# Kernel optimization log

Hardware: AMD Instinct MI355X
Metric: run time of the kernel (lower is better)

Reference implementation:

```python
import jax, jax.numpy as jnp
import numpy as np

B, C, H, W = 8, 64, 256, 256
EPS = 1e-5


def setup_inputs() -> dict:
    key = jax.random.key(0)
    ks = jax.random.split(key, 8)
    s = 1.0 / np.sqrt(C)
    return {
        "x": jax.random.normal(ks[0], (B, C, H, W), dtype=jnp.float32),
        "Wq": jax.random.uniform(ks[1], (C, C), jnp.float32, -s, s),
        "bq": jnp.zeros((C,), jnp.float32),
        "Wk": jax.random.uniform(ks[2], (C, C), jnp.float32, -s, s),
        "bk": jnp.zeros((C,), jnp.float32),
        "Wv": jax.random.uniform(ks[3], (C, C), jnp.float32, -s, s),
        "bv": jnp.zeros((C,), jnp.float32),
        "gamma": jnp.ones((C,), jnp.float32),
        "beta": jnp.zeros((C,), jnp.float32),
        "running_mean": jnp.zeros((C,), jnp.float32),
        "running_var": jnp.ones((C,), jnp.float32),
        "alpha": jnp.full((1,), 0.25, jnp.float32),  # PReLU single shared parameter
    }


def _conv1x1(x, w, b):
    # 1x1 conv == per-pixel channel mixing: [B,Ci,H,W] x [Co,Ci] -> [B,Co,H,W]
    return jnp.einsum("bihw,oi->bohw", x, w) + b[None, :, None, None]


def reference(x, Wq, bq, Wk, bk, Wv, bv, gamma, beta, running_mean, running_var, alpha):
    # d_k = sqrt(H); scores scaled by d_k**0.5 -> H**0.25 (faithful to source)
    scale = jnp.asarray(H, x.dtype) ** 0.25
    Q = _conv1x1(x, Wq, bq)
    K = _conv1x1(x, Wk, bk)
    V = _conv1x1(x, Wv, bv)
    # scores over spatial rows: [B,C,H,H]
    scores = jnp.einsum("bchw,bcgw->bchg", Q, K) / scale
    attn = jax.nn.softmax(scores, axis=-1)
    out = jnp.einsum("bchg,bcgw->bchw", attn, V)
    # BatchNorm2d (eval mode: running stats), then PReLU; dropout is identity in eval
    inv = gamma / jnp.sqrt(running_var + EPS)
    out = out * inv[None, :, None, None] + (beta - running_mean * inv)[None, :, None, None]
    a = alpha[0]
    out = jnp.where(out >= 0, out, a * out)
    return out
```

## Files before the change

kernel.cpp:

```cpp
#include <hip/hip_runtime.h>

#define B_ 8
#define C_ 64
#define H_ 256
#define W_ 256
#define HW_ 65536
#define PLANE_ 33554432

typedef __attribute__((ext_vector_type(8))) short short8;
typedef __attribute__((ext_vector_type(4))) float f32x4;
typedef __attribute__((ext_vector_type(4))) unsigned short ushort4v;

__device__ __forceinline__ unsigned short f2bf(float f){
  unsigned u = __float_as_uint(f);
  u += 0x7fffu + ((u >> 16) & 1u);
  return (unsigned short)(u >> 16);
}

__global__ __launch_bounds__(256, 4) void proj_kernel(
    const float* __restrict__ x,
    const float* __restrict__ Wq, const float* __restrict__ bq,
    const float* __restrict__ Wk, const float* __restrict__ bk,
    const float* __restrict__ Wv, const float* __restrict__ bv,
    unsigned short* __restrict__ Qb, unsigned short* __restrict__ Kb,
    unsigned short* __restrict__ Vb)
{
  __shared__ unsigned short lds[W_*64 + 64*64];
  unsigned short* Xt = lds;
  unsigned short* Wl = lds + W_*64;
  const int tid = threadIdx.x;
  const int lane = tid & 63;
  const int wv  = tid >> 6;
  const int q4 = lane >> 4, l16 = lane & 15;
  const int bid = blockIdx.x;
  const int b = bid >> 8, h = bid & 255;

  const float* wsrc[3] = {Wq, Wk, Wv};
  const float* bsrc[3] = {bq, bk, bv};

  const float* xb = x + (size_t)b*C_*HW_ + (size_t)h*W_;
  float4 xv[16];
  #pragma unroll
  for (int it=0; it<16; ++it){
    int i = it*4 + wv;
    xv[it] = *(const float4*)(xb + (size_t)i*HW_ + lane*4);
  }
  float4 w0v[4];
  #pragma unroll
  for (int k=0;k<4;++k){
    int idx4 = k*256 + tid;
    int o = idx4 >> 4, i4 = idx4 & 15;
    w0v[k] = *(const float4*)(Wq + o*64 + i4*4);
  }
  float biasr[3][4];
  #pragma unroll
  for (int p=0;p<3;++p)
    #pragma unroll
    for (int nf=0;nf<4;++nf)
      biasr[p][nf] = bsrc[p][nf*16 + l16];

  #pragma unroll
  for (int it=0; it<16; ++it){
    int i = it*4 + wv;
    float fv[4] = {xv[it].x, xv[it].y, xv[it].z, xv[it].w};
    #pragma unroll
    for (int k2=0;k2<4;++k2){
      int w = lane*4 + k2;
      int slot = (w&7) ^ ((w>>3)&7);
      Xt[w*64 + (i ^ (slot<<3))] = f2bf(fv[k2]);
    }
  }
  #pragma unroll
  for (int k=0;k<4;++k){
    int idx4 = k*256 + tid;
    int o = idx4 >> 4, i4 = idx4 & 15;
    ushort4v sv;
    sv[0]=f2bf(w0v[k].x); sv[1]=f2bf(w0v[k].y); sv[2]=f2bf(w0v[k].z); sv[3]=f2bf(w0v[k].w);
    *(ushort4v*)&Wl[o*64 + ((i4*4) ^ ((o&7)<<3))] = sv;
  }
  __syncthreads();

  short8 aX[4][2];
  #pragma unroll
  for (int mf=0;mf<4;++mf){
    int w = wv*64 + mf*16 + l16;
    int slot = (w&7) ^ ((w>>3)&7);
    #pragma unroll
    for (int kk=0;kk<2;++kk)
      aX[mf][kk] = *(const short8*)&Xt[w*64 + ((8*q4 + 32*kk) ^ (slot<<3))];
  }

  unsigned short* outp[3] = {Qb, Kb, Vb};
  const size_t obase = (size_t)b*C_*HW_ + (size_t)h*W_;
  unsigned short* Obuf = Xt;

  #pragma unroll
  for (int p=0;p<3;++p){
    ushort4v pk[4][4];
    #pragma unroll
    for (int nf=0;nf<4;++nf){
      const int o = nf*16 + l16;
      const int key = (o&7)<<3;
      short8 bW0 = *(const short8*)&Wl[o*64 + ((8*q4)      ^ key)];
      short8 bW1 = *(const short8*)&Wl[o*64 + ((8*q4 + 32) ^ key)];
      f32x4 acc[4];
      #pragma unroll
      for (int mf=0;mf<4;++mf){ f32x4 z={0.f,0.f,0.f,0.f}; acc[mf]=z; }
      #pragma unroll
      for (int mf=0;mf<4;++mf)
        acc[mf] = __builtin_amdgcn_mfma_f32_16x16x32_bf16(aX[mf][0], bW0, acc[mf], 0,0,0);
      #pragma unroll
      for (int mf=0;mf<4;++mf)
        acc[mf] = __builtin_amdgcn_mfma_f32_16x16x32_bf16(aX[mf][1], bW1, acc[mf], 0,0,0);
      const float bb = biasr[p][nf];
      #pragma unroll
      for (int mf=0;mf<4;++mf){
        ushort4v sv;
        #pragma unroll
        for (int r=0;r<4;++r) sv[r] = f2bf(acc[mf][r] + bb);
        pk[nf][mf] = sv;
      }
    }
    float4 wnv[4];
    if (p < 2){
      #pragma unroll
      for (int k=0;k<4;++k){
        int idx4 = k*256 + tid;
        int o = idx4 >> 4, i4 = idx4 & 15;
        wnv[k] = *(const float4*)(wsrc[p+1] + o*64 + i4*4);
      }
    }
    __syncthreads();

    #pragma unroll
    for (int nf=0;nf<4;++nf){
      const int o = nf*16 + l16;
      const int key = (o&7)<<3;
      #pragma unroll
      for (int mf=0;mf<4;++mf){
        int w4 = wv*16 + mf*4 + q4;
        *(ushort4v*)&Obuf[o*256 + ((w4 ^ key)<<2)] = pk[nf][mf];
      }
    }
    if (p < 2){
      #pragma unroll
      for (int k=0;k<4;++k){
        int idx4 = k*256 + tid;
        int o = idx4 >> 4, i4 = idx4 & 15;
        ushort4v sv;
        sv[0]=f2bf(wnv[k].x); sv[1]=f2bf(wnv[k].y); sv[2]=f2bf(wnv[k].z); sv[3]=f2bf(wnv[k].w);
        *(ushort4v*)&Wl[o*64 + ((i4*4) ^ ((o&7)<<3))] = sv;
      }
    }
    __syncthreads();

    unsigned short* op = outp[p];
    #pragma unroll
    for (int rr=0; rr<16; ++rr){
      const int o = wv*16 + rr;
      const int key = (o&7)<<3;
      ushort4v sv = *(const ushort4v*)&Obuf[o*256 + ((lane ^ key)<<2)];
      *(ushort4v*)&op[obase + (size_t)o*HW_ + lane*4] = sv;
    }
  }
}

__global__ __launch_bounds__(256) void transpose_v(unsigned short* __restrict__ Vb)
{
  const int pi[10] = {0,0,0,0,1,1,1,2,2,3};
  const int pj[10] = {0,1,2,3,1,2,3,2,3,3};
  __shared__ unsigned short tA[64*72];
  __shared__ unsigned short tB[64*72];
  int t = threadIdx.x;
  int bid = blockIdx.x;
  int bc = bid / 10, pr = bid - bc*10;
  int ti = pi[pr], tj = pj[pr];
  unsigned short* base = Vb + (size_t)bc*HW_;
  int diag = (ti == tj);
  #pragma unroll
  for (int k=0;k<2;++k){
    int flat = t + k*256;
    int i = flat >> 3, j = (flat & 7)*8;
    int4 va = *(const int4*)(base + (size_t)(ti*64+i)*256 + tj*64 + j);
    *(int4*)&tA[i*72 + j] = va;
    if (!diag){
      int4 vb2 = *(const int4*)(base + (size_t)(tj*64+i)*256 + ti*64 + j);
      *(int4*)&tB[i*72 + j] = vb2;
    }
  }
  __syncthreads();
  #pragma unroll
  for (int k=0;k<2;++k){
    int flat = t + k*256;
    int i = flat >> 3, j = (flat & 7)*8;
    int4 vo; unsigned short* po = (unsigned short*)&vo;
    #pragma unroll
    for (int e=0;e<8;++e) po[e] = tA[(j+e)*72 + i];
    *(int4*)(base + (size_t)(tj*64+i)*256 + ti*64 + j) = vo;
    if (!diag){
      int4 vo2; unsigned short* po2 = (unsigned short*)&vo2;
      #pragma unroll
      for (int e=0;e<8;++e) po2[e] = tB[(j+e)*72 + i];
      *(int4*)(base + (size_t)(ti*64+i)*256 + tj*64 + j) = vo2;
    }
  }
}

__device__ __forceinline__ int swzkey(int r){ return (r & 31) ^ ((r & 3) << 3); }

__device__ __forceinline__ void stage_tile(unsigned short* dst, const unsigned short* src, int tid){
  #pragma unroll
  for (int k=0;k<8;++k){
    int j = tid + k*256;
    int gj = j ^ swzkey(j >> 5);
    __builtin_amdgcn_global_load_lds(
      (const __attribute__((address_space(1))) void*)(src + (size_t)gj*8),
      (__attribute__((address_space(3))) void*)(dst + (size_t)j*8),
      16, 0, 0);
  }
}

__global__ __launch_bounds__(256) void attn_kernel(
    const unsigned short* __restrict__ Qb, const unsigned short* __restrict__ Kb,
    const unsigned short* __restrict__ Vtb,
    const float* __restrict__ gamma, const float* __restrict__ beta,
    const float* __restrict__ rmean, const float* __restrict__ rvar,
    const float* __restrict__ alphaP,
    float* __restrict__ out)
{
  __shared__ unsigned short s[64*256];
  const int tid = threadIdx.x;
  const int lane = tid & 63;
  const int wv = tid >> 6;
  const int q4 = lane >> 4, l16 = lane & 15;
  const int n = blockIdx.x;
  const int work = (n & 7)*256 + (n >> 3);
  const int bc = work >> 2, ht = work & 3;
  const int c = bc & 63;

  const unsigned short* Qp = Qb  + (size_t)bc*HW_ + (size_t)ht*64*W_;
  const unsigned short* Kp = Kb  + (size_t)bc*HW_;
  const unsigned short* Vp = Vtb + (size_t)bc*HW_;

  stage_tile(s, Kp, tid);

  short8 aq[8];
  {
    const int row = wv*16 + l16;
    #pragma unroll
    for (int kk=0;kk<8;++kk)
      aq[kk] = *(const short8*)(Qp + (size_t)row*W_ + 8*q4 + 32*kk);
  }

  f32x4 sa[16];
  #pragma unroll
  for (int f=0;f<16;++f){ f32x4 z={0.f,0.f,0.f,0.f}; sa[f]=z; }

  __syncthreads();
  #pragma unroll
  for (int gt=0; gt<4; ++gt){
    #pragma unroll
    for (int nf=0;nf<4;++nf){
      const int g = nf*16 + l16;
      const int ko = swzkey(g);
      const int f = gt*4 + nf;
      #pragma unroll
      for (int kk=0;kk<8;++kk){
        short8 bk_ = *(const short8*)&s[g*256 + (((q4 + 4*kk) ^ ko) << 3)];
        sa[f] = __builtin_amdgcn_mfma_f32_16x16x32_bf16(aq[kk], bk_, sa[f], 0,0,0);
      }
    }
    __syncthreads();
    if (gt < 3){
      stage_tile(s, Kp + (size_t)(gt+1)*64*W_, tid);
      __syncthreads();
    }
  }

  float mrow[4], rden[4];
  #pragma unroll
  for (int r=0;r<4;++r){
    float m = -3.0e38f;
    #pragma unroll
    for (int f=0;f<16;++f) m = fmaxf(m, sa[f][r]);
    m = fmaxf(m, __shfl_xor(m, 1, 16));
    m = fmaxf(m, __shfl_xor(m, 2, 16));
    m = fmaxf(m, __shfl_xor(m, 4, 16));
    m = fmaxf(m, __shfl_xor(m, 8, 16));
    mrow[r] = m;
  }
  const float cs = 0.25f * 1.4426950408889634f;
  float psum[4] = {0.f,0.f,0.f,0.f};
  #pragma unroll
  for (int f=0;f<16;++f){
    #pragma unroll
    for (int r=0;r<4;++r){
      float pv = exp2f((sa[f][r] - mrow[r]) * cs);
      sa[f][r] = pv;
      psum[r] += pv;
    }
  }
  #pragma unroll
  for (int r=0;r<4;++r){
    float ssum = psum[r];
    ssum += __shfl_xor(ssum, 1, 16);
    ssum += __shfl_xor(ssum, 2, 16);
    ssum += __shfl_xor(ssum, 4, 16);
    ssum += __shfl_xor(ssum, 8, 16);
    rden[r] = 1.0f / ssum;
  }

  #pragma unroll
  for (int r=0;r<4;++r){
    const int row = wv*16 + 4*q4 + r;
    const int ko = swzkey(row);
    #pragma unroll
    for (int f=0;f<16;++f){
      const int g2 = l16 + 16*f;
      s[row*256 + ((((g2>>3) ^ ko) << 3) | (g2 & 7))] = f2bf(sa[f][r] * rden[r]);
    }
  }
  __syncthreads();

  short8 pb[8];
  {
    const int row = wv*16 + l16;
    const int ko = swzkey(row);
    #pragma unroll
    for (int kk=0;kk<8;++kk)
      pb[kk] = *(const short8*)&s[row*256 + (((q4 + 4*kk) ^ ko) << 3)];
  }
  __syncthreads();

  f32x4 oa[16];
  #pragma unroll
  for (int f=0;f<16;++f){ f32x4 z={0.f,0.f,0.f,0.f}; oa[f]=z; }

  stage_tile(s, Vp, tid);
  __syncthreads();
  #pragma unroll
  for (int wt=0; wt<4; ++wt){
    #pragma unroll
    for (int nf=0;nf<4;++nf){
      const int wrow = nf*16 + l16;
      const int ko = swzkey(wrow);
      const int mw = wt*4 + nf;
      #pragma unroll
      for (int kk=0;kk<8;++kk){
        short8 av = *(const short8*)&s[wrow*256 + (((q4 + 4*kk) ^ ko) << 3)];
        oa[mw] = __builtin_amdgcn_mfma_f32_16x16x32_bf16(av, pb[kk], oa[mw], 0,0,0);
      }
    }
    __syncthreads();
    if (wt < 3){
      stage_tile(s, Vp + (size_t)(wt+1)*64*W_, tid);
      __syncthreads();
    }
  }

  const float inv   = gamma[c] / sqrtf(rvar[c] + 1e-5f);
  const float shift = beta[c] - rmean[c]*inv;
  const float al    = alphaP[0];
  float* ob = out + (size_t)bc*HW_ + (size_t)ht*64*W_;
  const int hrow = wv*16 + l16;
  #pragma unroll
  for (int mw=0; mw<16; ++mw){
    f32x4 v;
    #pragma unroll
    for (int r=0;r<4;++r){
      float t = oa[mw][r]*inv + shift;
      v[r] = (t >= 0.f) ? t : al*t;
    }
    *(f32x4*)&ob[(size_t)hrow*W_ + mw*16 + 4*q4] = v;
  }
}

extern "C" void kernel_launch(void* const* d_in, const int* in_sizes, int n_in,
                              void* d_out, int out_size, void* d_ws, size_t ws_size,
                              hipStream_t stream)
{
  const float* x     = (const float*)d_in[0];
  const float* Wq    = (const float*)d_in[1];
  const float* bq    = (const float*)d_in[2];
  const float* Wk    = (const float*)d_in[3];
  const float* bk    = (const float*)d_in[4];
  const float* Wv    = (const float*)d_in[5];
  const float* bv    = (const float*)d_in[6];
  const float* gamma = (const float*)d_in[7];
  const float* beta  = (const float*)d_in[8];
  const float* rmean = (const float*)d_in[9];
  const float* rvar  = (const float*)d_in[10];
  const float* alpha = (const float*)d_in[11];
  float* out = (float*)d_out;

  unsigned short* Qb = (unsigned short*)d_ws;
  unsigned short* Kb = Qb + (size_t)PLANE_;
  unsigned short* Vb = Kb + (size_t)PLANE_;

  proj_kernel<<<B_*H_, 256, 0, stream>>>(x, Wq,bq, Wk,bk, Wv,bv, Qb, Kb, Vb);
  transpose_v<<<B_*C_*10, 256, 0, stream>>>(Vb);
  attn_kernel<<<B_*C_*4, 256, 0, stream>>>(Qb, Kb, Vb, gamma, beta, rmean, rvar, alpha, out);
}
```

Measured before the change: 423.7 us.

## Load x directly into LDS as fp32 and write projections straight to global

The projection kernel now uses global_load_lds to copy x rows into a 64KB fp32 LDS buffer instead of staging them through registers and converting to a transposed bf16 layout. The bf16 conversion moves to the MFMA operand gather, which uses strided scalar LDS reads. Output tiles are written directly from the MFMA accumulators to global memory, skipping the LDS transpose buffer, which removes syncs but leaves 8-byte scattered stores. The larger LDS footprint also lowers the occupancy hint from 4 to 2 blocks per CU.

```diff
diff --git a/kernel.cpp b/kernel.cpp
--- a/kernel.cpp
+++ b/kernel.cpp
@@ -17,7 +17,7 @@
   return (unsigned short)(u >> 16);
 }
 
-__global__ __launch_bounds__(256, 4) void proj_kernel(
+__global__ __launch_bounds__(256, 2) void proj_kernel(
     const float* __restrict__ x,
     const float* __restrict__ Wq, const float* __restrict__ bq,
     const float* __restrict__ Wk, const float* __restrict__ bk,
@@ -25,9 +25,8 @@
     unsigned short* __restrict__ Qb, unsigned short* __restrict__ Kb,
     unsigned short* __restrict__ Vb)
 {
-  __shared__ unsigned short lds[W_*64 + 64*64];
-  unsigned short* Xt = lds;
-  unsigned short* Wl = lds + W_*64;
+  __shared__ float Xf[64*256];
+  __shared__ unsigned short Wl[64*64];
   const int tid = threadIdx.x;
   const int lane = tid & 63;
   const int wv  = tid >> 6;
@@ -37,14 +36,19 @@
 
   const float* wsrc[3] = {Wq, Wk, Wv};
   const float* bsrc[3] = {bq, bk, bv};
-
   const float* xb = x + (size_t)b*C_*HW_ + (size_t)h*W_;
-  float4 xv[16];
-  #pragma unroll
-  for (int it=0; it<16; ++it){
-    int i = it*4 + wv;
-    xv[it] = *(const float4*)(xb + (size_t)i*HW_ + lane*4);
-  }
+
+  #pragma unroll
+  for (int k=0;k<16;++k){
+    int f = k*256 + tid;
+    int i = f >> 6;
+    int c = f & 63;
+    __builtin_amdgcn_global_load_lds(
+      (const __attribute__((address_space(1))) void*)(xb + (size_t)i*HW_ + c*4),
+      (__attribute__((address_space(3))) void*)(Xf + (size_t)f*4),
+      16, 0, 0);
+  }
+
   float4 w0v[4];
   #pragma unroll
   for (int k=0;k<4;++k){
@@ -59,17 +63,6 @@
     for (int nf=0;nf<4;++nf)
       biasr[p][nf] = bsrc[p][nf*16 + l16];
 
-  #pragma unroll
-  for (int it=0; it<16; ++it){
-    int i = it*4 + wv;
-    float fv[4] = {xv[it].x, xv[it].y, xv[it].z, xv[it].w};
-    #pragma unroll
-    for (int k2=0;k2<4;++k2){
-      int w = lane*4 + k2;
-      int slot = (w&7) ^ ((w>>3)&7);
-      Xt[w*64 + (i ^ (slot<<3))] = f2bf(fv[k2]);
-    }
-  }
   #pragma unroll
   for (int k=0;k<4;++k){
     int idx4 = k*256 + tid;
@@ -83,20 +76,33 @@
   short8 aX[4][2];
   #pragma unroll
   for (int mf=0;mf<4;++mf){
-    int w = wv*64 + mf*16 + l16;
-    int slot = (w&7) ^ ((w>>3)&7);
-    #pragma unroll
-    for (int kk=0;kk<2;++kk)
-      aX[mf][kk] = *(const short8*)&Xt[w*64 + ((8*q4 + 32*kk) ^ (slot<<3))];
+    const int w = wv*64 + mf*16 + l16;
+    #pragma unroll
+    for (int kk=0;kk<2;++kk){
+      const int i0 = 8*q4 + 32*kk;
+      short8 t;
+      #pragma unroll
+      for (int e=0;e<8;++e)
+        t[e] = (short)f2bf(Xf[(i0+e)*256 + w]);
+      aX[mf][kk] = t;
+    }
   }
 
   unsigned short* outp[3] = {Qb, Kb, Vb};
   const size_t obase = (size_t)b*C_*HW_ + (size_t)h*W_;
-  unsigned short* Obuf = Xt;
 
   #pragma unroll
   for (int p=0;p<3;++p){
-    ushort4v pk[4][4];
+    unsigned short* op = outp[p];
+    float4 wnv[4];
+    if (p < 2){
+      #pragma unroll
+      for (int k=0;k<4;++k){
+        int idx4 = k*256 + tid;
+        int o = idx4 >> 4, i4 = idx4 & 15;
+        wnv[k] = *(const float4*)(wsrc[p+1] + o*64 + i4*4);
+      }
+    }
     #pragma unroll
     for (int nf=0;nf<4;++nf){
       const int o = nf*16 + l16;
@@ -118,31 +124,11 @@
         ushort4v sv;
         #pragma unroll
         for (int r=0;r<4;++r) sv[r] = f2bf(acc[mf][r] + bb);
-        pk[nf][mf] = sv;
-      }
-    }
-    float4 wnv[4];
+        *(ushort4v*)&op[obase + (size_t)o*HW_ + (wv*64 + mf*16 + 4*q4)] = sv;
+      }
+    }
     if (p < 2){
-      #pragma unroll
-      for (int k=0;k<4;++k){
-        int idx4 = k*256 + tid;
-        int o = idx4 >> 4, i4 = idx4 & 15;
-        wnv[k] = *(const float4*)(wsrc[p+1] + o*64 + i4*4);
-      }
-    }
-    __syncthreads();
-
-    #pragma unroll
-    for (int nf=0;nf<4;++nf){
-      const int o = nf*16 + l16;
-      const int key = (o&7)<<3;
-      #pragma unroll
-      for (int mf=0;mf<4;++mf){
-        int w4 = wv*16 + mf*4 + q4;
-        *(ushort4v*)&Obuf[o*256 + ((w4 ^ key)<<2)] = pk[nf][mf];
-      }
-    }
-    if (p < 2){
+      __syncthreads();
       #pragma unroll
       for (int k=0;k<4;++k){
         int idx4 = k*256 + tid;
@@ -151,16 +137,7 @@
         sv[0]=f2bf(wnv[k].x); sv[1]=f2bf(wnv[k].y); sv[2]=f2bf(wnv[k].z); sv[3]=f2bf(wnv[k].w);
         *(ushort4v*)&Wl[o*64 + ((i4*4) ^ ((o&7)<<3))] = sv;
       }
-    }
-    __syncthreads();
-
-    unsigned short* op = outp[p];
-    #pragma unroll
-    for (int rr=0; rr<16; ++rr){
-      const int o = wv*16 + rr;
-      const int key = (o&7)<<3;
-      ushort4v sv = *(const ushort4v*)&Obuf[o*256 + ((lane ^ key)<<2)];
-      *(ushort4v*)&op[obase + (size_t)o*HW_ + lane*4] = sv;
+      __syncthreads();
     }
   }
 }
```

Result: faster. 409.1 us (-3.4%).
